# Kernel tuning notes

Hardware: AMD Instinct MI355X
Metric: run time of the kernel (lower is better)

The kernel has to match this reference:

```python
import jax, jax.numpy as jnp
import numpy as np
from jax import lax

STRIDE = 1
DILATION = 1


def setup_inputs() -> dict:
    key = jax.random.key(0)
    k1, k2 = jax.random.split(key)
    inp = jax.random.normal(k1, (16, 1, 512, 512), dtype=jnp.float32)   # [B, 1, H, W]
    weight = jax.random.normal(k2, (16, 32, 9, 9), dtype=jnp.float32)   # [B, J, k, k]
    return {"input": inp, "weight": weight}


def reference(input, weight):
    # Original: for each (batch i, out-channel j), conv2d(input[i:i+1], weight[i,j][None,None]).
    # Equivalent fused form: grouped conv with groups = B, one 1-channel group per sample.
    B, J, kh, kw = weight.shape
    _, Cin, H, W = input.shape  # Cin == 1 (required by the per-slice conv math)
    pad = kw // 2 - 1  # self.padding == 0 -> int(k/2) - 1 rule in forward
    x = input.reshape(1, B * Cin, H, W)           # [1, B, H, W]
    w = weight.reshape(B * J, 1, kh, kw)          # [B*J, 1, k, k]
    out = lax.conv_general_dilated(
        x, w,
        window_strides=(STRIDE, STRIDE),
        padding=[(pad, pad), (pad, pad)],
        rhs_dilation=(DILATION, DILATION),
        feature_group_count=B,
        dimension_numbers=("NCHW", "OIHW", "NCHW"),
    )  # [1, B*J, H', W']
    return out.reshape(B, J, out.shape[2], out.shape[3])
```

## Files before the change

### kernel.cpp

```cpp
#include <hip/hip_runtime.h>

#define BB  16
#define JJ  32
#define HH  512
#define WW  512
#define KK  9
#define PAD 3
#define OH  510
#define OW  510

#define RROWS  4
#define NRAW   12
#define IN_DW  268
#define IN_PITCH_B (IN_DW * 4)
#define IN_BYTES (NRAW * IN_PITCH_B)

#define D_PITCH 524
#define DBUF_OFF IN_BYTES
#define LDS_BYTES (DBUF_OFF + 16 * D_PITCH * 4)

#define WRAW_OFF DBUF_OFF

typedef __bf16 bf16x8 __attribute__((ext_vector_type(8)));
typedef float  f32x4  __attribute__((ext_vector_type(4)));

__device__ __forceinline__ unsigned pack2bf(float a, float b) {
    unsigned ua = __float_as_uint(a) + 0x8000u;
    unsigned ub = __float_as_uint(b) + 0x8000u;
    return (ua >> 16) | (ub & 0xFFFF0000u);
}

__device__ __forceinline__ void barrier_lds_only() {
    asm volatile("s_waitcnt lgkmcnt(0)" ::: "memory");
    __builtin_amdgcn_s_barrier();
}

__global__ __launch_bounds__(256, 3)
void conv_mfma_kernel(const float* __restrict__ in,
                      const float* __restrict__ wgt,
                      float* __restrict__ out) {
    __shared__ __align__(16) char lds[LDS_BYTES];

    const int tid  = threadIdx.x;
    const int lane = tid & 63;
    const int w    = tid >> 6;
    const int c    = lane & 15;
    const int q    = lane >> 4;
    const int g    = q >> 1;
    const int h    = q & 1;
    const int par  = w >> 1;

    const int id  = blockIdx.x;
    const int xcd = id & 7;
    const int wk  = xcd * 512 + (id >> 3);
    const int yt  = wk & 127;
    const int p   = wk >> 7;
    const int jg  = p & 1;
    const int bi  = p >> 1;
    const int y0  = yt * RROWS;

    {
        const uint4 z = make_uint4(0u, 0u, 0u, 0u);
        for (int idx = tid; idx < 800; idx += 256)
            *(uint4*)(lds + WRAW_OFF + idx * 16) = z;
    }
    __syncthreads();

    float* rawF = (float*)(lds + WRAW_OFF);
    const float* wB = wgt + (size_t)(bi * JJ + jg * 16) * (KK * KK);
    for (int idx = tid; idx < 16 * 81; idx += 256) {
        const int j   = idx / 81;
        const int rem = idx - j * 81;
        const int u   = rem / 9;
        const int v   = rem - u * 9;
        rawF[j * 200 + u * 20 + v + 1] = wB[idx];
    }
    __syncthreads();

    bf16x8 afrag[5];
    #pragma unroll
    for (int s = 0; s < 5; ++s) {
        const int u = 2 * s + g;
        const int base = c * 200 + u * 20 + 8 * h + par;
        float wv[8];
        #pragma unroll
        for (int e = 0; e < 8; ++e) wv[e] = rawF[base + e];
        const uint4 pk = make_uint4(pack2bf(wv[0], wv[1]), pack2bf(wv[2], wv[3]),
                                    pack2bf(wv[4], wv[5]), pack2bf(wv[6], wv[7]));
        afrag[s] = __builtin_bit_cast(bf16x8, pk);
    }

    const float* inB = in + (size_t)bi * (HH * WW);
    #pragma unroll 1
    for (int idx = tid; idx < NRAW * 66; idx += 256) {
        const int rr = idx / 66;
        const int m  = idx - rr * 66;
        const int gr = y0 - PAD + rr;
        float el[8];
        if ((unsigned)gr < (unsigned)HH) {
            const float* rp = inB + gr * WW + 8 * m - 4;
            if (m >= 1 && m <= 63) {
                const float4 a = *(const float4*)rp;
                const float4 b = *(const float4*)(rp + 4);
                el[0]=a.x; el[1]=a.y; el[2]=a.z; el[3]=a.w;
                el[4]=b.x; el[5]=b.y; el[6]=b.z; el[7]=b.w;
            } else {
                #pragma unroll
                for (int t = 0; t < 8; ++t) {
                    const int gx = 8 * m - 4 + t;
                    el[t] = ((unsigned)gx < (unsigned)WW) ? rp[t] : 0.f;
                }
            }
        } else {
            #pragma unroll
            for (int t = 0; t < 8; ++t) el[t] = 0.f;
        }
        *(uint4*)(lds + rr * IN_PITCH_B + m * 16) =
            make_uint4(pack2bf(el[0], el[1]), pack2bf(el[2], el[3]),
                       pack2bf(el[4], el[5]), pack2bf(el[6], el[7]));
    }
    __syncthreads();

    const uint* L = (const uint*)lds;
    const int dwl = c + par + 4 * h + 128 * (w & 1);
    float* D = (float*)(lds + DBUF_OFF);
    const int xb = 256 * (w & 1) + 2 * c + par;
    const size_t plane = (size_t)OH * OW;
    float* outB = out + (size_t)(bi * JJ + jg * 16) * plane;

    #pragma unroll 1
    for (int r = 0; r < RROWS; ++r) {
        f32x4 acc[8];
        #pragma unroll
        for (int i = 0; i < 8; ++i) acc[i] = (f32x4){0.f, 0.f, 0.f, 0.f};

        #pragma unroll
        for (int s = 0; s < 5; ++s) {
            int u = 2 * s + g;
            if (u > 8) u = 0;
            const int rowdw = (r + u) * IN_DW + dwl;
            #pragma unroll
            for (int i = 0; i < 8; ++i) {
                const int d = rowdw + 16 * i;
                const uint4 bf = make_uint4(L[d], L[d + 1], L[d + 2], L[d + 3]);
                acc[i] = __builtin_amdgcn_mfma_f32_16x16x32_bf16(
                             afrag[s], __builtin_bit_cast(bf16x8, bf), acc[i], 0, 0, 0);
            }
        }

        #pragma unroll
        for (int i = 0; i < 8; ++i) {
            const int x = xb + 32 * i;
            #pragma unroll
            for (int rg = 0; rg < 4; ++rg)
                D[(q * 4 + rg) * D_PITCH + x] = acc[i][rg];
        }
        barrier_lds_only();

        const int y = y0 + r;
        if (y < OH) {
            #pragma unroll
            for (int jj = 0; jj < 4; ++jj) {
                const int jl = w * 4 + jj;
                float* op = outB + (size_t)jl * plane + (size_t)y * OW;
                #pragma unroll
                for (int seg = 0; seg < 4; ++seg) {
                    const int px = seg * 128 + 2 * lane;
                    if (px + 1 < OW)
                        *(float2*)(op + px) = *(const float2*)&D[jl * D_PITCH + px];
                }
            }
        }
        barrier_lds_only();
    }
}

extern "C" void kernel_launch(void* const* d_in, const int* in_sizes, int n_in,
                              void* d_out, int out_size, void* d_ws, size_t ws_size,
                              hipStream_t stream) {
    const float* inp = (const float*)d_in[0];
    const float* wgt = (const float*)d_in[1];
    float* out = (float*)d_out;

    conv_mfma_kernel<<<dim3(4096), 256, 0, stream>>>(inp, wgt, out);
}
```

Measured before the change: 145.4 us.

## Compute all 32 output channels per block to reuse input tile

Each block now covers all 32 output channels of a sample instead of 16, which halves the grid. Every bf16 input fragment read from LDS now feeds two MFMAs, one per 16-channel weight group. This removes the duplicated global input loads and bf16 conversion that came from two blocks staging the same rows, and it also changes the store mapping to one float2 per thread across 16 channels. In exchange it doubles the accumulator registers and adds two extra LDS staging passes and barriers per row, which may reduce occupancy or overlap in what is mostly a write-bound kernel.

```diff
diff --git a/kernel.cpp b/kernel.cpp
--- a/kernel.cpp
+++ b/kernel.cpp
@@ -52,23 +52,21 @@
 
     const int id  = blockIdx.x;
     const int xcd = id & 7;
-    const int wk  = xcd * 512 + (id >> 3);
+    const int wk  = xcd * 256 + (id >> 3);
     const int yt  = wk & 127;
-    const int p   = wk >> 7;
-    const int jg  = p & 1;
-    const int bi  = p >> 1;
+    const int bi  = wk >> 7;
     const int y0  = yt * RROWS;
 
     {
         const uint4 z = make_uint4(0u, 0u, 0u, 0u);
-        for (int idx = tid; idx < 800; idx += 256)
+        for (int idx = tid; idx < 1600; idx += 256)
             *(uint4*)(lds + WRAW_OFF + idx * 16) = z;
     }
     __syncthreads();
 
     float* rawF = (float*)(lds + WRAW_OFF);
-    const float* wB = wgt + (size_t)(bi * JJ + jg * 16) * (KK * KK);
-    for (int idx = tid; idx < 16 * 81; idx += 256) {
+    const float* wB = wgt + (size_t)bi * JJ * (KK * KK);
+    for (int idx = tid; idx < JJ * 81; idx += 256) {
         const int j   = idx / 81;
         const int rem = idx - j * 81;
         const int u   = rem / 9;
@@ -77,17 +75,20 @@
     }
     __syncthreads();
 
-    bf16x8 afrag[5];
+    bf16x8 afrag[5][2];
     #pragma unroll
     for (int s = 0; s < 5; ++s) {
         const int u = 2 * s + g;
-        const int base = c * 200 + u * 20 + 8 * h + par;
-        float wv[8];
-        #pragma unroll
-        for (int e = 0; e < 8; ++e) wv[e] = rawF[base + e];
-        const uint4 pk = make_uint4(pack2bf(wv[0], wv[1]), pack2bf(wv[2], wv[3]),
-                                    pack2bf(wv[4], wv[5]), pack2bf(wv[6], wv[7]));
-        afrag[s] = __builtin_bit_cast(bf16x8, pk);
+        #pragma unroll
+        for (int jt = 0; jt < 2; ++jt) {
+            const int base = (jt * 16 + c) * 200 + u * 20 + 8 * h + par;
+            float wv[8];
+            #pragma unroll
+            for (int e = 0; e < 8; ++e) wv[e] = rawF[base + e];
+            const uint4 pk = make_uint4(pack2bf(wv[0], wv[1]), pack2bf(wv[2], wv[3]),
+                                        pack2bf(wv[4], wv[5]), pack2bf(wv[6], wv[7]));
+            afrag[s][jt] = __builtin_bit_cast(bf16x8, pk);
+        }
     }
 
     const float* inB = in + (size_t)bi * (HH * WW);
@@ -126,13 +127,17 @@
     float* D = (float*)(lds + DBUF_OFF);
     const int xb = 256 * (w & 1) + 2 * c + par;
     const size_t plane = (size_t)OH * OW;
-    float* outB = out + (size_t)(bi * JJ + jg * 16) * plane;
+    float* outB = out + (size_t)bi * JJ * plane;
+    const int px = 2 * tid;
 
     #pragma unroll 1
     for (int r = 0; r < RROWS; ++r) {
-        f32x4 acc[8];
-        #pragma unroll
-        for (int i = 0; i < 8; ++i) acc[i] = (f32x4){0.f, 0.f, 0.f, 0.f};
+        f32x4 acc0[8], acc1[8];
+        #pragma unroll
+        for (int i = 0; i < 8; ++i) {
+            acc0[i] = (f32x4){0.f, 0.f, 0.f, 0.f};
+            acc1[i] = (f32x4){0.f, 0.f, 0.f, 0.f};
+        }
 
         #pragma unroll
         for (int s = 0; s < 5; ++s) {
@@ -142,34 +147,44 @@
             #pragma unroll
             for (int i = 0; i < 8; ++i) {
                 const int d = rowdw + 16 * i;
-                const uint4 bf = make_uint4(L[d], L[d + 1], L[d + 2], L[d + 3]);
-                acc[i] = __builtin_amdgcn_mfma_f32_16x16x32_bf16(
-                             afrag[s], __builtin_bit_cast(bf16x8, bf), acc[i], 0, 0, 0);
+                const uint4 bv = make_uint4(L[d], L[d + 1], L[d + 2], L[d + 3]);
+                const bf16x8 bf = __builtin_bit_cast(bf16x8, bv);
+                acc0[i] = __builtin_amdgcn_mfma_f32_16x16x32_bf16(afrag[s][0], bf, acc0[i], 0, 0, 0);
+                acc1[i] = __builtin_amdgcn_mfma_f32_16x16x32_bf16(afrag[s][1], bf, acc1[i], 0, 0, 0);
             }
         }
+
+        const int y = y0 + r;
 
         #pragma unroll
         for (int i = 0; i < 8; ++i) {
             const int x = xb + 32 * i;
             #pragma unroll
             for (int rg = 0; rg < 4; ++rg)
-                D[(q * 4 + rg) * D_PITCH + x] = acc[i][rg];
-        }
-        barrier_lds_only();
-
-        const int y = y0 + r;
-        if (y < OH) {
-            #pragma unroll
-            for (int jj = 0; jj < 4; ++jj) {
-                const int jl = w * 4 + jj;
-                float* op = outB + (size_t)jl * plane + (size_t)y * OW;
-                #pragma unroll
-                for (int seg = 0; seg < 4; ++seg) {
-                    const int px = seg * 128 + 2 * lane;
-                    if (px + 1 < OW)
-                        *(float2*)(op + px) = *(const float2*)&D[jl * D_PITCH + px];
-                }
-            }
+                D[(q * 4 + rg) * D_PITCH + x] = acc0[i][rg];
+        }
+        barrier_lds_only();
+        if (y < OH && px + 1 < OW) {
+            float* op = outB + (size_t)y * OW + px;
+            #pragma unroll
+            for (int jj = 0; jj < 16; ++jj)
+                *(float2*)(op + (size_t)jj * plane) = *(const float2*)&D[jj * D_PITCH + px];
+        }
+        barrier_lds_only();
+
+        #pragma unroll
+        for (int i = 0; i < 8; ++i) {
+            const int x = xb + 32 * i;
+            #pragma unroll
+            for (int rg = 0; rg < 4; ++rg)
+                D[(q * 4 + rg) * D_PITCH + x] = acc1[i][rg];
+        }
+        barrier_lds_only();
+        if (y < OH && px + 1 < OW) {
+            float* op = outB + (size_t)(16) * plane + (size_t)y * OW + px;
+            #pragma unroll
+            for (int jj = 0; jj < 16; ++jj)
+                *(float2*)(op + (size_t)jj * plane) = *(const float2*)&D[jj * D_PITCH + px];
         }
         barrier_lds_only();
     }
@@ -182,5 +197,5 @@
     const float* wgt = (const float*)d_in[1];
     float* out = (float*)d_out;
 
-    conv_mfma_kernel<<<dim3(4096), 256, 0, stream>>>(inp, wgt, out);
-}
+    conv_mfma_kernel<<<dim3(2048), 256, 0, stream>>>(inp, wgt, out);
+}
```

New measurement: 154.3 us. +6.1%, slower.

## Keep all row accumulators in registers and store output directly without LDS staging

Applied to the files above, without the earlier changes.

Rather than staging each output row through an LDS buffer and writing coalesced float2 stores after barriers, the kernel now keeps accumulators for all four rows in registers (128 floats per thread) and writes scalar floats straight to global memory. This removes the per-row LDS round-trip and the two barriers per row, and launch bounds drop to 2 blocks per SM to leave room for the extra registers. In exchange, the global stores become strided scalar writes, with adjacent lanes two floats apart and partial wave coverage, which can hurt write coalescing on a kernel dominated by output writes. Occupancy also falls.

```diff
diff --git a/kernel.cpp b/kernel.cpp
--- a/kernel.cpp
+++ b/kernel.cpp
@@ -15,11 +15,8 @@
 #define IN_PITCH_B (IN_DW * 4)
 #define IN_BYTES (NRAW * IN_PITCH_B)
 
-#define D_PITCH 524
-#define DBUF_OFF IN_BYTES
-#define LDS_BYTES (DBUF_OFF + 16 * D_PITCH * 4)
-
-#define WRAW_OFF DBUF_OFF
+#define WRAW_OFF IN_BYTES
+#define LDS_BYTES (WRAW_OFF + 16 * 200 * 4)
 
 typedef __bf16 bf16x8 __attribute__((ext_vector_type(8)));
 typedef float  f32x4  __attribute__((ext_vector_type(4)));
@@ -30,12 +27,7 @@
     return (ua >> 16) | (ub & 0xFFFF0000u);
 }
 
-__device__ __forceinline__ void barrier_lds_only() {
-    asm volatile("s_waitcnt lgkmcnt(0)" ::: "memory");
-    __builtin_amdgcn_s_barrier();
-}
-
-__global__ __launch_bounds__(256, 3)
+__global__ __launch_bounds__(256, 2)
 void conv_mfma_kernel(const float* __restrict__ in,
                       const float* __restrict__ wgt,
                       float* __restrict__ out) {
@@ -75,20 +67,6 @@
         const int v   = rem - u * 9;
         rawF[j * 200 + u * 20 + v + 1] = wB[idx];
     }
-    __syncthreads();
-
-    bf16x8 afrag[5];
-    #pragma unroll
-    for (int s = 0; s < 5; ++s) {
-        const int u = 2 * s + g;
-        const int base = c * 200 + u * 20 + 8 * h + par;
-        float wv[8];
-        #pragma unroll
-        for (int e = 0; e < 8; ++e) wv[e] = rawF[base + e];
-        const uint4 pk = make_uint4(pack2bf(wv[0], wv[1]), pack2bf(wv[2], wv[3]),
-                                    pack2bf(wv[4], wv[5]), pack2bf(wv[6], wv[7]));
-        afrag[s] = __builtin_bit_cast(bf16x8, pk);
-    }
 
     const float* inB = in + (size_t)bi * (HH * WW);
     #pragma unroll 1
@@ -121,19 +99,31 @@
     }
     __syncthreads();
 
+    bf16x8 afrag[5];
+    #pragma unroll
+    for (int s = 0; s < 5; ++s) {
+        const int u = 2 * s + g;
+        const int base = c * 200 + u * 20 + 8 * h + par;
+        float wv[8];
+        #pragma unroll
+        for (int e = 0; e < 8; ++e) wv[e] = rawF[base + e];
+        const uint4 pk = make_uint4(pack2bf(wv[0], wv[1]), pack2bf(wv[2], wv[3]),
+                                    pack2bf(wv[4], wv[5]), pack2bf(wv[6], wv[7]));
+        afrag[s] = __builtin_bit_cast(bf16x8, pk);
+    }
+
     const uint* L = (const uint*)lds;
     const int dwl = c + par + 4 * h + 128 * (w & 1);
-    float* D = (float*)(lds + DBUF_OFF);
-    const int xb = 256 * (w & 1) + 2 * c + par;
-    const size_t plane = (size_t)OH * OW;
-    float* outB = out + (size_t)(bi * JJ + jg * 16) * plane;
 
-    #pragma unroll 1
+    f32x4 acc[RROWS][8];
+    #pragma unroll
+    for (int r = 0; r < RROWS; ++r)
+        #pragma unroll
+        for (int i = 0; i < 8; ++i)
+            acc[r][i] = (f32x4){0.f, 0.f, 0.f, 0.f};
+
+    #pragma unroll
     for (int r = 0; r < RROWS; ++r) {
-        f32x4 acc[8];
-        #pragma unroll
-        for (int i = 0; i < 8; ++i) acc[i] = (f32x4){0.f, 0.f, 0.f, 0.f};
-
         #pragma unroll
         for (int s = 0; s < 5; ++s) {
             int u = 2 * s + g;
@@ -142,36 +132,34 @@
             #pragma unroll
             for (int i = 0; i < 8; ++i) {
                 const int d = rowdw + 16 * i;
-                const uint4 bf = make_uint4(L[d], L[d + 1], L[d + 2], L[d + 3]);
-                acc[i] = __builtin_amdgcn_mfma_f32_16x16x32_bf16(
-                             afrag[s], __builtin_bit_cast(bf16x8, bf), acc[i], 0, 0, 0);
+                const uint4 bv = make_uint4(L[d], L[d + 1], L[d + 2], L[d + 3]);
+                acc[r][i] = __builtin_amdgcn_mfma_f32_16x16x32_bf16(
+                                afrag[s], __builtin_bit_cast(bf16x8, bv),
+                                acc[r][i], 0, 0, 0);
             }
         }
+    }
 
+    const int xb = 256 * (w & 1) + 2 * c + par;
+    const size_t plane = (size_t)OH * OW;
+    float* outB = out + (size_t)(bi * JJ + jg * 16) * plane;
+
+    #pragma unroll
+    for (int rg = 0; rg < 4; ++rg) {
+        const int jl = q * 4 + rg;
+        float* opl = outB + (size_t)jl * plane;
         #pragma unroll
-        for (int i = 0; i < 8; ++i) {
-            const int x = xb + 32 * i;
-            #pragma unroll
-            for (int rg = 0; rg < 4; ++rg)
-                D[(q * 4 + rg) * D_PITCH + x] = acc[i][rg];
-        }
-        barrier_lds_only();
-
-        const int y = y0 + r;
-        if (y < OH) {
-            #pragma unroll
-            for (int jj = 0; jj < 4; ++jj) {
-                const int jl = w * 4 + jj;
-                float* op = outB + (size_t)jl * plane + (size_t)y * OW;
+        for (int r = 0; r < RROWS; ++r) {
+            const int y = y0 + r;
+            if (y < OH) {
+                float* orow = opl + (size_t)y * OW;
                 #pragma unroll
-                for (int seg = 0; seg < 4; ++seg) {
-                    const int px = seg * 128 + 2 * lane;
-                    if (px + 1 < OW)
-                        *(float2*)(op + px) = *(const float2*)&D[jl * D_PITCH + px];
+                for (int i = 0; i < 8; ++i) {
+                    const int px = xb + 32 * i;
+                    if (px < OW) orow[px] = acc[r][i][rg];
                 }
             }
         }
-        barrier_lds_only();
     }
 }
 
```

Result: slower. 194.6 us (+33.8%).
